# Kernel optimization log

Measured on AMD Instinct MI355X. Metric: run time of the kernel, lower is better.

The kernel has to match this reference:

```python
import jax, jax.numpy as jnp
import numpy as np

GORDER = 8
IN_DIM = 32768
CLASSES = 10
BATCH = 2048
THETA = 2.0 * np.pi / GORDER  # group-angle scale
OUT_SCALE = 1.0 / (IN_DIM ** 0.5)


def round_ste(x):
    # FastRound: round in fwd, identity gradient (straight-through)
    return x + jax.lax.stop_gradient(jnp.round(x) - x)


def setup_inputs() -> dict:
    key = jax.random.key(0)
    k1, k2 = jax.random.split(key)
    x = jax.random.normal(k1, (BATCH, IN_DIM), dtype=jnp.float32)
    weight = jax.random.normal(k2, (CLASSES, IN_DIM), dtype=jnp.float32)
    radius = jnp.ones((1,), dtype=jnp.float32)
    return {"x": x, "weight": weight, "radius": radius}


def reference(x, weight, radius):
    # Eval-mode forward: weight_q = round(weight) (STE), then GroupSim.
    # GroupSim: sum_i radius * (cos(tw)cos(tx) + sin(tw)sin(tx))
    # collapsed into two dense GEMMs instead of a [B,out,in,2] broadcast.
    w_q = round_ste(weight)
    tw = THETA * w_q          # [out, in]
    tx = THETA * x            # [B, in]
    sims = radius[0] * (jnp.cos(tx) @ jnp.cos(tw).T + jnp.sin(tx) @ jnp.sin(tw).T)  # [B, out]
    return sims * OUT_SCALE
```

## Files before the change

kernel.cpp:

```cpp
#include <hip/hip_runtime.h>

typedef float v2f __attribute__((ext_vector_type(2)));
typedef unsigned int v2u __attribute__((ext_vector_type(2)));

#define IN_DIM 32768
#define BATCH 2048
#define CLASSES 10
#define NC 2
#define RB 4
#define TPB 256
#define VEC 2
#define COLS_PER_CHUNK (IN_DIM / NC)
#define COLS_PER_J (TPB * VEC)
#define JITER (COLS_PER_CHUNK / COLS_PER_J)
#define OUT_SCALE 0.005524271728019903f
#define LDS_STRIDE 41

__global__ __launch_bounds__(256) void build_table(const float* __restrict__ w,
                                                   unsigned int* __restrict__ idx) {
    int c = blockIdx.x * blockDim.x + threadIdx.x;
    if (c >= IN_DIM) return;
    unsigned int d = 0;
#pragma unroll
    for (int o = 0; o < CLASSES; ++o) {
        int k = ((int)rintf(w[(size_t)o * IN_DIM + c])) & 7;
        d |= (unsigned int)k << (3 * o);
    }
    idx[c] = d;
}

__device__ __forceinline__ void body(v2u pidx, const v2f* xc,
                                     const v2f* lutC, const v2f* lutS,
                                     v2f acc[RB][5]) {
    v2f ck0[5], sk0[5], ck1[5], sk1[5];
#pragma unroll
    for (int p = 0; p < 5; ++p) {
        unsigned int a = (pidx.x >> (6 * p)) & 63;
        unsigned int b = (pidx.y >> (6 * p)) & 63;
        ck0[p] = lutC[a]; sk0[p] = lutS[a];
        ck1[p] = lutC[b]; sk1[p] = lutS[b];
    }
#pragma unroll
    for (int r = 0; r < RB; ++r) {
        float cx0 = __builtin_amdgcn_cosf(xc[r].x * 0.125f);
        float sx0 = __builtin_amdgcn_sinf(xc[r].x * 0.125f);
        float cx1 = __builtin_amdgcn_cosf(xc[r].y * 0.125f);
        float sx1 = __builtin_amdgcn_sinf(xc[r].y * 0.125f);
        v2f c0 = {cx0, cx0}, s0 = {sx0, sx0};
        v2f c1 = {cx1, cx1}, s1 = {sx1, sx1};
#pragma unroll
        for (int p = 0; p < 5; ++p) {
            acc[r][p] = __builtin_elementwise_fma(
                c0, ck0[p], __builtin_elementwise_fma(s0, sk0[p], acc[r][p]));
            acc[r][p] = __builtin_elementwise_fma(
                c1, ck1[p], __builtin_elementwise_fma(s1, sk1[p], acc[r][p]));
        }
    }
}

#define LOADBUF(XB, IB, CO)                                                    \
    do {                                                                       \
        IB = *(const v2u*)(ibase + (CO));                                      \
        _Pragma("unroll")                                                      \
        for (int r = 0; r < RB; ++r)                                           \
            XB[r] = *(const v2f*)(xbase + (size_t)r * IN_DIM + (CO));          \
    } while (0)

__global__ __launch_bounds__(256, 4) void gsim_main(const float* __restrict__ x,
                                                    const unsigned int* __restrict__ idx,
                                                    float* __restrict__ part) {
    __shared__ v2f lutC[64], lutS[64];
    __shared__ float lds[128][LDS_STRIDE];
    const int chunk = blockIdx.x % NC;
    const int rowblk = blockIdx.x / NC;
    const int tid = threadIdx.x;
    const int row0 = rowblk * RB;
    const int cbase = chunk * COLS_PER_CHUNK;
    const int jstart = (blockIdx.x * 13) & (JITER - 1);

    if (tid < 64) {
        lutC[tid] = (v2f){__builtin_amdgcn_cosf((tid & 7) * 0.125f),
                          __builtin_amdgcn_cosf((tid >> 3) * 0.125f)};
        lutS[tid] = (v2f){__builtin_amdgcn_sinf((tid & 7) * 0.125f),
                          __builtin_amdgcn_sinf((tid >> 3) * 0.125f)};
    }
    __syncthreads();

    v2f acc[RB][5];
#pragma unroll
    for (int r = 0; r < RB; ++r)
#pragma unroll
        for (int p = 0; p < 5; ++p) acc[r][p] = (v2f){0.f, 0.f};

    const float* xbase = x + (size_t)row0 * IN_DIM + cbase + VEC * tid;
    const unsigned int* ibase = idx + cbase + VEC * tid;

    v2f xA[RB], xB[RB];
    v2u iA, iB;
    LOADBUF(xA, iA, ((jstart) & (JITER - 1)) * COLS_PER_J);
    LOADBUF(xB, iB, ((jstart + 1) & (JITER - 1)) * COLS_PER_J);

    for (int t = 0; t + 2 < JITER; t += 2) {
        body(iA, xA, lutC, lutS, acc);
        LOADBUF(xA, iA, ((jstart + t + 2) & (JITER - 1)) * COLS_PER_J);

        body(iB, xB, lutC, lutS, acc);
        LOADBUF(xB, iB, ((jstart + t + 3) & (JITER - 1)) * COLS_PER_J);
    }
    body(iA, xA, lutC, lutS, acc);
    body(iB, xB, lutC, lutS, acc);

    const float* af = (const float*)acc;
    if (tid >= 128) {
#pragma unroll
        for (int v = 0; v < RB * CLASSES; ++v)
            lds[tid - 128][v] = af[v];
    }
    __syncthreads();
    if (tid < 128) {
#pragma unroll
        for (int v = 0; v < RB * CLASSES; ++v)
            lds[tid][v] = af[v] + lds[tid][v];
    }
    __syncthreads();
    if (tid < RB * CLASSES) {
        float s = 0.f;
        for (int t = 0; t < 128; ++t) s += lds[t][tid];
        part[(size_t)chunk * (BATCH * CLASSES) + (size_t)row0 * CLASSES + tid] = s;
    }
}

__global__ __launch_bounds__(256) void reduce_out(const float* __restrict__ part,
                                                  const float* __restrict__ radius,
                                                  float* __restrict__ out) {
    int i = blockIdx.x * blockDim.x + threadIdx.x;
    if (i >= BATCH * CLASSES) return;
    float s = 0.f;
#pragma unroll
    for (int c = 0; c < NC; ++c) s += part[(size_t)c * (BATCH * CLASSES) + i];
    out[i] = s * radius[0] * OUT_SCALE;
}

extern "C" void kernel_launch(void* const* d_in, const int* in_sizes, int n_in,
                              void* d_out, int out_size, void* d_ws, size_t ws_size,
                              hipStream_t stream) {
    const float* x = (const float*)d_in[0];
    const float* w = (const float*)d_in[1];
    const float* radius = (const float*)d_in[2];
    float* out = (float*)d_out;

    unsigned int* tab = (unsigned int*)d_ws;
    float* part = (float*)((char*)d_ws + (size_t)IN_DIM * sizeof(unsigned int));

    build_table<<<IN_DIM / 256, 256, 0, stream>>>(w, tab);
    gsim_main<<<(BATCH / RB) * NC, 256, 0, stream>>>(x, tab, part);
    reduce_out<<<(BATCH * CLASSES + 255) / 256, 256, 0, stream>>>(part, radius, out);
}
```

Baseline: 62.10 us.

## Stage x tiles into LDS via async global_load_lds double buffering

Replaces the per-thread register double-buffered loads of x with direct global-to-LDS async loads (global_load_lds, 16 bytes per lane), one wave per row, into a two-slot LDS buffer. Each iteration prefetches the next tile while computing on the current one and ends with a block barrier. This aims to cut register pressure and issue wider loads, but adds a __syncthreads per iteration. It also relies on the barrier to cover the async LDS writes, with no explicit vmcnt wait, which may be a correctness risk.

```diff
diff --git a/kernel.cpp b/kernel.cpp
--- a/kernel.cpp
+++ b/kernel.cpp
@@ -58,25 +58,34 @@
     }
 }
 
-#define LOADBUF(XB, IB, CO)                                                    \
-    do {                                                                       \
-        IB = *(const v2u*)(ibase + (CO));                                      \
-        _Pragma("unroll")                                                      \
-        for (int r = 0; r < RB; ++r)                                           \
-            XB[r] = *(const v2f*)(xbase + (size_t)r * IN_DIM + (CO));          \
-    } while (0)
-
 __global__ __launch_bounds__(256, 4) void gsim_main(const float* __restrict__ x,
                                                     const unsigned int* __restrict__ idx,
                                                     float* __restrict__ part) {
+    __shared__ float xlds[2][RB][COLS_PER_J];
     __shared__ v2f lutC[64], lutS[64];
     __shared__ float lds[128][LDS_STRIDE];
     const int chunk = blockIdx.x % NC;
     const int rowblk = blockIdx.x / NC;
     const int tid = threadIdx.x;
+    const int wv = tid >> 6;
+    const int ln = tid & 63;
     const int row0 = rowblk * RB;
     const int cbase = chunk * COLS_PER_CHUNK;
     const int jstart = (blockIdx.x * 13) & (JITER - 1);
+
+#define STAGE(BUF, CO)                                                         \
+    do {                                                                       \
+        const float* g0 = x + (size_t)(row0 + wv) * IN_DIM + cbase + (CO) +    \
+                          ln * 4;                                              \
+        __builtin_amdgcn_global_load_lds(                                      \
+            (const __attribute__((address_space(1))) unsigned int*)g0,         \
+            (__attribute__((address_space(3))) unsigned int*)&xlds[BUF][wv][0],\
+            16, 0, 0);                                                         \
+        __builtin_amdgcn_global_load_lds(                                      \
+            (const __attribute__((address_space(1))) unsigned int*)(g0 + 256), \
+            (__attribute__((address_space(3))) unsigned int*)&xlds[BUF][wv][256],\
+            16, 0, 0);                                                         \
+    } while (0)
 
     if (tid < 64) {
         lutC[tid] = (v2f){__builtin_amdgcn_cosf((tid & 7) * 0.125f),
@@ -84,7 +93,6 @@
         lutS[tid] = (v2f){__builtin_amdgcn_sinf((tid & 7) * 0.125f),
                           __builtin_amdgcn_sinf((tid >> 3) * 0.125f)};
     }
-    __syncthreads();
 
     v2f acc[RB][5];
 #pragma unroll
@@ -92,23 +100,32 @@
 #pragma unroll
         for (int p = 0; p < 5; ++p) acc[r][p] = (v2f){0.f, 0.f};
 
-    const float* xbase = x + (size_t)row0 * IN_DIM + cbase + VEC * tid;
     const unsigned int* ibase = idx + cbase + VEC * tid;
 
-    v2f xA[RB], xB[RB];
-    v2u iA, iB;
-    LOADBUF(xA, iA, ((jstart) & (JITER - 1)) * COLS_PER_J);
-    LOADBUF(xB, iB, ((jstart + 1) & (JITER - 1)) * COLS_PER_J);
+    const int co0 = jstart * COLS_PER_J;
+    STAGE(0, co0);
+    v2u iA = *(const v2u*)(ibase + co0);
+    __syncthreads();
 
-    for (int t = 0; t + 2 < JITER; t += 2) {
-        body(iA, xA, lutC, lutS, acc);
-        LOADBUF(xA, iA, ((jstart + t + 2) & (JITER - 1)) * COLS_PER_J);
-
-        body(iB, xB, lutC, lutS, acc);
-        LOADBUF(xB, iB, ((jstart + t + 3) & (JITER - 1)) * COLS_PER_J);
+    int buf = 0;
+#pragma unroll 1
+    for (int t = 0; t < JITER; ++t) {
+        v2u iN = iA;
+        if (t + 1 < JITER) {
+            const int con = ((jstart + t + 1) & (JITER - 1)) * COLS_PER_J;
+            STAGE(buf ^ 1, con);
+            iN = *(const v2u*)(ibase + con);
+        }
+        v2f xr[RB];
+#pragma unroll
+        for (int r = 0; r < RB; ++r)
+            xr[r] = *(const v2f*)&xlds[buf][r][VEC * tid];
+        body(iA, xr, lutC, lutS, acc);
+        __syncthreads();
+        buf ^= 1;
+        iA = iN;
     }
-    body(iA, xA, lutC, lutS, acc);
-    body(iB, xB, lutC, lutS, acc);
+#undef STAGE
 
     const float* af = (const float*)acc;
     if (tid >= 128) {
```

Result: slower. 72.85 us (+17.3%).
